# Kernel tuning notes

Measured on AMD Instinct MI355X. Metric: run time of the kernel, lower is better.

The kernel has to match this reference:

```python
import jax, jax.numpy as jnp
import numpy as np

T, D, H = 2048, 256, 256
DISCOUNT = 0.99
LAMBDA = 0.9
CONT_ALPHA = 0.01


def setup_inputs() -> dict:
    key = jax.random.key(0)
    ks = jax.random.split(key, 5)
    xs = jax.random.normal(ks[0], (T, D), jnp.float32)
    gs = jax.random.normal(ks[1], (T,), jnp.float32)            # returns / targets
    dones = (jax.random.uniform(ks[2], (T,)) < 0.02).astype(jnp.float32)  # sparse episode ends
    ys = jnp.stack([gs, dones], axis=1)                          # [T, 2] as in train_step
    W1 = jax.random.normal(ks[3], (D, H), jnp.float32) * (1.0 / float(np.sqrt(D)))
    b1 = jnp.zeros((H,), jnp.float32)
    W2 = jax.random.normal(ks[4], (H, 1), jnp.float32) * (1.0 / float(np.sqrt(H)))
    b2 = jnp.zeros((1,), jnp.float32)
    return {"xs": xs, "ys": ys, "W1": W1, "b1": b1, "W2": W2, "b2": b2}


def _value(params, x):
    # Value network: self(x)[0] for a batch of 1 -> scalar prediction.
    W1, b1, W2, b2 = params
    h = jax.nn.relu(x @ W1 + b1)          # [H]
    return (h @ W2 + b2)[0]               # scalar us


def _td_lambda(xs, ys, W1, b1, W2, b2):
    params = (W1, b1, W2, b2)
    gs, dones = ys[:, 0], ys[:, 1]
    zeros = tuple(jnp.zeros_like(p) for p in params)
    val_grad = jax.value_and_grad(_value)

    def step(carry, inp):
        z, total, r = carry
        x, g, done = inp
        us, grads = val_grad(params, x)   # grads of the PREDICTION us, as in tape.gradient(us, vars)
        error = (g - us) ** 2             # compiled_loss (MSE) on a single sample
        sigma = error - r                 # continuing TD error
        r = r + CONT_ALPHA * sigma
        # eligibility trace update and accumulated update
        z = tuple(DISCOUNT * LAMBDA * zi + gi for zi, gi in zip(z, grads))
        total = tuple(ti - sigma * zi for ti, zi in zip(total, z))
        # episode reset: zero traces and average-reward estimate when done
        keep = 1.0 - (done > 0.5).astype(jnp.float32)
        z = tuple(zi * keep for zi in z)
        r = r * keep
        return (z, total, r), sigma

    init = (zeros, zeros, jnp.float32(0.0))
    (_, total, _), sigmas = jax.lax.scan(step, init, (xs, gs, dones))
    # accumulated gradients for all trainable vars (flattened) + final sigma (reported loss)
    return jnp.concatenate([t.ravel() for t in total] + [sigmas[-1][None]])


def reference(xs, ys, W1, b1, W2, b2):
    return _td_lambda(xs, ys, W1, b1, W2, b2)
```

## Files before the change

kernel.cpp:

```cpp
#include <hip/hip_runtime.h>

#define GL  0.891f
#define OMA 0.99f
#define AL  0.01f

#define OFF_H   0
#define OFF_U   524288
#define OFF_PW1 526336
#define OFF_PB1 2623488
#define OFF_PW2 2631680
#define WS_FLOATS 2639872

__global__ __launch_bounds__(512, 2) void fwd_kernel(
    const float* __restrict__ xs, const float* __restrict__ W1,
    const float* __restrict__ b1, const float* __restrict__ W2,
    const float* __restrict__ b2,
    float* __restrict__ Hbuf, float* __restrict__ u) {
  const int tid = threadIdx.x;
  const int j = tid & 255;
  const int half = tid >> 8;
  const int r0 = blockIdx.x * 8;
  __shared__ __align__(16) float xsl[8 * 260];
  __shared__ __align__(16) float red[8][256];

  {
    const int row = tid >> 6;
    const int k0 = (tid & 63) * 4;
    float4 v = *reinterpret_cast<const float4*>(&xs[(r0 + row) * 256 + k0]);
    *reinterpret_cast<float4*>(&xsl[row * 260 + k0]) = v;
  }

  const int kb = half * 128;
  float wcur[16], wnxt[16];
#pragma unroll
  for (int kk = 0; kk < 16; ++kk)
    wcur[kk] = W1[(kb + kk) * 256 + j];
  __syncthreads();

  float acc[8] = {0.f, 0.f, 0.f, 0.f, 0.f, 0.f, 0.f, 0.f};
#pragma unroll
  for (int b = 0; b < 8; ++b) {
    if (b < 7) {
#pragma unroll
      for (int kk = 0; kk < 16; ++kk)
        wnxt[kk] = W1[(kb + (b + 1) * 16 + kk) * 256 + j];
    }
    const int k = kb + b * 16;
#pragma unroll
    for (int r = 0; r < 8; ++r) {
#pragma unroll
      for (int q = 0; q < 4; ++q) {
        const float4 xv = *reinterpret_cast<const float4*>(&xsl[r * 260 + k + 4 * q]);
        acc[r] = fmaf(xv.x, wcur[4 * q + 0], acc[r]);
        acc[r] = fmaf(xv.y, wcur[4 * q + 1], acc[r]);
        acc[r] = fmaf(xv.z, wcur[4 * q + 2], acc[r]);
        acc[r] = fmaf(xv.w, wcur[4 * q + 3], acc[r]);
      }
    }
#pragma unroll
    for (int kk = 0; kk < 16; ++kk) wcur[kk] = wnxt[kk];
  }

  if (half == 0) {
#pragma unroll
    for (int r = 0; r < 8; ++r) red[r][j] = acc[r];
  }
  __syncthreads();
  if (half == 1) {
    const float bj = b1[j];
    const float w2j = W2[j];
#pragma unroll
    for (int r = 0; r < 8; ++r) {
      const float a = red[r][j] + acc[r] + bj;
      const float h = fmaxf(a, 0.f);
      Hbuf[(r0 + r) * 256 + j] = h;
      red[r][j] = h * w2j;
    }
  }
  __syncthreads();
  for (int s = 128; s >= 1; s >>= 1) {
    if (j < s) {
#pragma unroll
      for (int rr = 0; rr < 4; ++rr)
        red[half * 4 + rr][j] += red[half * 4 + rr][j + s];
    }
    __syncthreads();
  }
  if (half == 0 && j < 8) u[r0 + j] = red[j][0] + b2[0];
}

__global__ __launch_bounds__(256, 4) void scan_w1_kernel(
    const float* __restrict__ u, const float* __restrict__ ys,
    const float* __restrict__ xs, const float* __restrict__ Hbuf,
    const float* __restrict__ W2,
    float* __restrict__ pW1, float* __restrict__ pB1, float* __restrict__ pW2,
    float* __restrict__ outp) {
  const int tid = threadIdx.x;
  const int blk = blockIdx.x;
  const int dc = blk >> 5;
  const int kc = blk & 31;
  const int d0 = dc * 32;
  const int tb = kc * 64;
  const int lane = tid & 63;
  const int w = tid >> 6;
  const int th = tid >> 7;
  const int j0 = tid & 127;
  const int tsl = th * 32;

  __shared__ __align__(16) float LDS[8704];
  float* xt = LDS;
  float* c_l = LDS + 2048;
  __shared__ float aggA[4], aggB[4], ag2A[4], ag2B[4], wsum[4];

#pragma unroll
  for (int q = 0; q < 2; ++q) {
    const int idx = tid * 2 + q;
    const int row = idx >> 3;
    const int qd = idx & 7;
    *reinterpret_cast<float4*>(&xt[row * 32 + qd * 4]) =
        *reinterpret_cast<const float4*>(&xs[(tb + row) * 256 + d0 + qd * 4]);
  }

  float hcur[16], hnxt[16];
#pragma unroll
  for (int i = 0; i < 8; ++i) {
    hcur[2 * i + 0] = Hbuf[(tb + tsl + i) * 256 + j0];
    hcur[2 * i + 1] = Hbuf[(tb + tsl + i) * 256 + j0 + 128];
  }

  float e[8], kp[8];
  {
    const float4 ua = ((const float4*)u)[2 * tid];
    const float4 ub = ((const float4*)u)[2 * tid + 1];
    const float uu[8] = {ua.x, ua.y, ua.z, ua.w, ub.x, ub.y, ub.z, ub.w};
#pragma unroll
    for (int q = 0; q < 4; ++q) {
      const float4 y = ((const float4*)ys)[4 * tid + q];
      float da = y.x - uu[2 * q];
      float db = y.z - uu[2 * q + 1];
      e[2 * q] = da * da;
      e[2 * q + 1] = db * db;
      kp[2 * q] = (y.y > 0.5f) ? 0.f : 1.f;
      kp[2 * q + 1] = (y.w > 0.5f) ? 0.f : 1.f;
    }
  }
  float A = 1.f, B = 0.f;
#pragma unroll
  for (int i = 0; i < 8; ++i) {
    const float a = kp[i] * OMA;
    B = fmaf(a, B, kp[i] * (AL * e[i]));
    A *= a;
  }
#pragma unroll
  for (int s = 1; s < 64; s <<= 1) {
    const float pA = __shfl_up(A, s, 64);
    const float pB = __shfl_up(B, s, 64);
    if (lane >= s) { B = fmaf(A, pB, B); A *= pA; }
  }
  if (lane == 63) { aggA[w] = A; aggB[w] = B; }
  __syncthreads();
  float rin;
  {
    float rw = 0.f;
    for (int v = 0; v < w; ++v) rw = fmaf(aggA[v], rw, aggB[v]);
    float lA = __shfl_up(A, 1, 64);
    float lB = __shfl_up(B, 1, 64);
    if (lane == 0) { lA = 1.f; lB = 0.f; }
    rin = fmaf(lA, rw, lB);
  }
  float sig[8];
  {
    float r = rin;
#pragma unroll
    for (int i = 0; i < 8; ++i) {
      sig[i] = e[i] - r;
      const float a = kp[i] * OMA;
      r = fmaf(a, r, kp[i] * (AL * e[i]));
    }
  }
  if (blk == 0 && tid == 255) outp[66049] = sig[7];

  float A2 = 1.f, B2 = 0.f;
#pragma unroll
  for (int i = 7; i >= 0; --i) {
    const float a = GL * kp[i];
    B2 = fmaf(a, B2, -sig[i]);
    A2 *= a;
  }
#pragma unroll
  for (int s = 1; s < 64; s <<= 1) {
    const float nA = __shfl_down(A2, s, 64);
    const float nB = __shfl_down(B2, s, 64);
    if (lane + s < 64) { B2 = fmaf(A2, nB, B2); A2 *= nA; }
  }
  if (lane == 0) { ag2A[w] = A2; ag2B[w] = B2; }
  __syncthreads();
  float cin;
  {
    float cw = 0.f;
    for (int v = 3; v > w; --v) cw = fmaf(ag2A[v], cw, ag2B[v]);
    float lA = __shfl_down(A2, 1, 64);
    float lB = __shfl_down(B2, 1, 64);
    if (lane == 63) { lA = 1.f; lB = 0.f; }
    cin = fmaf(lA, cw, lB);
  }
  float cr[8];
  float cc = cin, csum = 0.f;
#pragma unroll
  for (int i = 7; i >= 0; --i) {
    cc = fmaf(GL * kp[i], cc, -sig[i]);
    cr[i] = cc;
    csum += cc;
  }
  *reinterpret_cast<float4*>(&c_l[8 * tid]) = make_float4(cr[0], cr[1], cr[2], cr[3]);
  *reinterpret_cast<float4*>(&c_l[8 * tid + 4]) = make_float4(cr[4], cr[5], cr[6], cr[7]);
  if (blk == 0) {
#pragma unroll
    for (int s = 32; s >= 1; s >>= 1) csum += __shfl_xor(csum, s, 64);
    if (lane == 0) wsum[w] = csum;
  }
  __syncthreads();
  if (blk == 0 && tid == 0)
    outp[66048] = wsum[0] + wsum[1] + wsum[2] + wsum[3];

  const float w2a = W2[j0];
  const float w2b = W2[j0 + 128];
  float acc0[32], acc1[32];
#pragma unroll
  for (int d = 0; d < 32; ++d) { acc0[d] = 0.f; acc1[d] = 0.f; }
  float sb0 = 0.f, sb1 = 0.f, sw0 = 0.f, sw1 = 0.f;
  const bool do_bw = (dc == 0);

#pragma unroll
  for (int b = 0; b < 4; ++b) {
    if (b < 3) {
#pragma unroll
      for (int i = 0; i < 8; ++i) {
        hnxt[2 * i + 0] = Hbuf[(tb + tsl + (b + 1) * 8 + i) * 256 + j0];
        hnxt[2 * i + 1] = Hbuf[(tb + tsl + (b + 1) * 8 + i) * 256 + j0 + 128];
      }
    }
#pragma unroll
    for (int i = 0; i < 8; ++i) {
      const int tl = tsl + b * 8 + i;
      const float ct = c_l[tb + tl];
      const float h0 = hcur[2 * i + 0];
      const float h1 = hcur[2 * i + 1];
      const float gc0 = (h0 > 0.f) ? w2a * ct : 0.f;
      const float gc1 = (h1 > 0.f) ? w2b * ct : 0.f;
      if (do_bw) {
        sb0 += gc0; sb1 += gc1;
        sw0 = fmaf(ct, h0, sw0); sw1 = fmaf(ct, h1, sw1);
      }
#pragma unroll
      for (int q = 0; q < 8; ++q) {
        const float4 xv = *reinterpret_cast<const float4*>(&xt[tl * 32 + 4 * q]);
        acc0[4 * q + 0] = fmaf(gc0, xv.x, acc0[4 * q + 0]);
        acc0[4 * q + 1] = fmaf(gc0, xv.y, acc0[4 * q + 1]);
        acc0[4 * q + 2] = fmaf(gc0, xv.z, acc0[4 * q + 2]);
        acc0[4 * q + 3] = fmaf(gc0, xv.w, acc0[4 * q + 3]);
        acc1[4 * q + 0] = fmaf(gc1, xv.x, acc1[4 * q + 0]);
        acc1[4 * q + 1] = fmaf(gc1, xv.y, acc1[4 * q + 1]);
        acc1[4 * q + 2] = fmaf(gc1, xv.z, acc1[4 * q + 2]);
        acc1[4 * q + 3] = fmaf(gc1, xv.w, acc1[4 * q + 3]);
      }
    }
#pragma unroll
    for (int kk = 0; kk < 16; ++kk) hcur[kk] = hnxt[kk];
  }

  __syncthreads();
  if (th == 0) {
#pragma unroll
    for (int d = 0; d < 32; ++d) {
      LDS[(0 * 32 + d) * 128 + j0] = acc0[d];
      LDS[(32 + d) * 128 + j0] = acc1[d];
    }
    if (do_bw) {
      LDS[8192 + j0] = sb0;
      LDS[8192 + 128 + j0] = sb1;
      LDS[8448 + j0] = sw0;
      LDS[8448 + 128 + j0] = sw1;
    }
  }
  __syncthreads();
  if (th == 1) {
#pragma unroll
    for (int d = 0; d < 32; ++d) {
      pW1[kc * 65536 + (d0 + d) * 256 + j0] = LDS[d * 128 + j0] + acc0[d];
      pW1[kc * 65536 + (d0 + d) * 256 + j0 + 128] = LDS[(32 + d) * 128 + j0] + acc1[d];
    }
    if (do_bw) {
      pB1[kc * 256 + j0] = LDS[8192 + j0] + sb0;
      pB1[kc * 256 + j0 + 128] = LDS[8192 + 128 + j0] + sb1;
      pW2[kc * 256 + j0] = LDS[8448 + j0] + sw0;
      pW2[kc * 256 + j0 + 128] = LDS[8448 + 128 + j0] + sw1;
    }
  }
}

__global__ __launch_bounds__(256) void reduce_kernel(
    const float* __restrict__ pW1, const float* __restrict__ pB1,
    const float* __restrict__ pW2, float* __restrict__ outp) {
  if (blockIdx.x < 256) {
    const int col = blockIdx.x * 256 + threadIdx.x;
    float v[32];
#pragma unroll
    for (int k = 0; k < 32; ++k) v[k] = pW1[k * 65536 + col];
    float s = 0.f;
#pragma unroll
    for (int k = 0; k < 32; ++k) s += v[k];
    outp[col] = s;
  } else {
    const int j = threadIdx.x;
    float b[32], c[32];
#pragma unroll
    for (int k = 0; k < 32; ++k) { b[k] = pB1[k * 256 + j]; c[k] = pW2[k * 256 + j]; }
    float sb = 0.f, sw = 0.f;
#pragma unroll
    for (int k = 0; k < 32; ++k) { sb += b[k]; sw += c[k]; }
    outp[65536 + j] = sb;
    outp[65792 + j] = sw;
  }
}

extern "C" void kernel_launch(void* const* d_in, const int* in_sizes, int n_in,
                              void* d_out, int out_size, void* d_ws, size_t ws_size,
                              hipStream_t stream) {
  const float* xs = (const float*)d_in[0];
  const float* ys = (const float*)d_in[1];
  const float* W1 = (const float*)d_in[2];
  const float* b1 = (const float*)d_in[3];
  const float* W2 = (const float*)d_in[4];
  const float* b2 = (const float*)d_in[5];
  float* outp = (float*)d_out;
  float* ws = (float*)d_ws;

  if (ws_size < (size_t)WS_FLOATS * sizeof(float)) return;

  float* Hbuf = ws + OFF_H;
  float* ubuf = ws + OFF_U;
  float* pW1  = ws + OFF_PW1;
  float* pB1  = ws + OFF_PB1;
  float* pW2  = ws + OFF_PW2;

  fwd_kernel<<<256, 512, 0, stream>>>(xs, W1, b1, W2, b2, Hbuf, ubuf);
  scan_w1_kernel<<<256, 256, 0, stream>>>(ubuf, ys, xs, Hbuf, W2,
                                          pW1, pB1, pW2, outp);
  reduce_kernel<<<257, 256, 0, stream>>>(pW1, pB1, pW2, outp);
}
```

Baseline: 33.39 us.

## Repartition W1-gradient over output tiles and drop partial-sum reduce kernel

The scan/outer-product kernel now assigns each block a 16x16 tile of the W1 gradient and loops over all 2048 timesteps, instead of splitting time across blocks and writing 32 partial copies. The per-block results are reduced in-block with shuffles and LDS and written straight to the output. This removes the third reduce kernel and the large partial-sum workspace traffic. The cost is that every block reruns the full scan over all timesteps and streams xs and Hbuf over the whole time range from global memory without LDS staging.

```diff
diff --git a/kernel.cpp b/kernel.cpp
--- a/kernel.cpp
+++ b/kernel.cpp
@@ -4,12 +4,9 @@
 #define OMA 0.99f
 #define AL  0.01f
 
-#define OFF_H   0
-#define OFF_U   524288
-#define OFF_PW1 526336
-#define OFF_PB1 2623488
-#define OFF_PW2 2631680
-#define WS_FLOATS 2639872
+#define OFF_H 0
+#define OFF_U 524288
+#define WS_FLOATS 526336
 
 __global__ __launch_bounds__(512, 2) void fwd_kernel(
     const float* __restrict__ xs, const float* __restrict__ W1,
@@ -89,55 +86,41 @@
   if (half == 0 && j < 8) u[r0 + j] = red[j][0] + b2[0];
 }
 
-__global__ __launch_bounds__(256, 4) void scan_w1_kernel(
+__global__ __launch_bounds__(512, 2) void scan_w1_kernel(
     const float* __restrict__ u, const float* __restrict__ ys,
     const float* __restrict__ xs, const float* __restrict__ Hbuf,
-    const float* __restrict__ W2,
-    float* __restrict__ pW1, float* __restrict__ pB1, float* __restrict__ pW2,
-    float* __restrict__ outp) {
+    const float* __restrict__ W2, float* __restrict__ outp) {
   const int tid = threadIdx.x;
   const int blk = blockIdx.x;
-  const int dc = blk >> 5;
-  const int kc = blk & 31;
-  const int d0 = dc * 32;
-  const int tb = kc * 64;
+  const int dcb = blk >> 4;
+  const int jc = blk & 15;
+  const int d0 = dcb * 16;
+  const int j0 = jc * 16;
+  const int jj = tid & 15;
+  const int tt = tid >> 4;
   const int lane = tid & 63;
   const int w = tid >> 6;
-  const int th = tid >> 7;
-  const int j0 = tid & 127;
-  const int tsl = th * 32;
-
-  __shared__ __align__(16) float LDS[8704];
-  float* xt = LDS;
-  float* c_l = LDS + 2048;
-  __shared__ float aggA[4], aggB[4], ag2A[4], ag2B[4], wsum[4];
-
-#pragma unroll
-  for (int q = 0; q < 2; ++q) {
-    const int idx = tid * 2 + q;
-    const int row = idx >> 3;
-    const int qd = idx & 7;
-    *reinterpret_cast<float4*>(&xt[row * 32 + qd * 4]) =
-        *reinterpret_cast<const float4*>(&xs[(tb + row) * 256 + d0 + qd * 4]);
-  }
-
-  float hcur[16], hnxt[16];
-#pragma unroll
-  for (int i = 0; i < 8; ++i) {
-    hcur[2 * i + 0] = Hbuf[(tb + tsl + i) * 256 + j0];
-    hcur[2 * i + 1] = Hbuf[(tb + tsl + i) * 256 + j0 + 128];
-  }
-
-  float e[8], kp[8];
-  {
-    const float4 ua = ((const float4*)u)[2 * tid];
-    const float4 ub = ((const float4*)u)[2 * tid + 1];
-    const float uu[8] = {ua.x, ua.y, ua.z, ua.w, ub.x, ub.y, ub.z, ub.w};
-#pragma unroll
-    for (int q = 0; q < 4; ++q) {
-      const float4 y = ((const float4*)ys)[4 * tid + q];
-      float da = y.x - uu[2 * q];
-      float db = y.z - uu[2 * q + 1];
+
+  __shared__ __align__(16) float c_l[2048];
+  __shared__ float red[8][16][20];
+  __shared__ float aggA[8], aggB[8], ag2A[8], ag2B[8], wsum[8];
+
+  const float w2j = W2[j0 + jj];
+
+  float hA[8], hB[8];
+#pragma unroll
+  for (int i = 0; i < 8; ++i)
+    hA[i] = Hbuf[(i * 32 + tt) * 256 + j0 + jj];
+
+  float e[4], kp[4];
+  {
+    const float4 u4 = ((const float4*)u)[tid];
+    const float uu[4] = {u4.x, u4.y, u4.z, u4.w};
+#pragma unroll
+    for (int q = 0; q < 2; ++q) {
+      const float4 y = ((const float4*)ys)[2 * tid + q];
+      const float da = y.x - uu[2 * q];
+      const float db = y.z - uu[2 * q + 1];
       e[2 * q] = da * da;
       e[2 * q + 1] = db * db;
       kp[2 * q] = (y.y > 0.5f) ? 0.f : 1.f;
@@ -146,7 +129,7 @@
   }
   float A = 1.f, B = 0.f;
 #pragma unroll
-  for (int i = 0; i < 8; ++i) {
+  for (int i = 0; i < 4; ++i) {
     const float a = kp[i] * OMA;
     B = fmaf(a, B, kp[i] * (AL * e[i]));
     A *= a;
@@ -168,21 +151,21 @@
     if (lane == 0) { lA = 1.f; lB = 0.f; }
     rin = fmaf(lA, rw, lB);
   }
-  float sig[8];
+  float sig[4];
   {
     float r = rin;
 #pragma unroll
-    for (int i = 0; i < 8; ++i) {
+    for (int i = 0; i < 4; ++i) {
       sig[i] = e[i] - r;
       const float a = kp[i] * OMA;
       r = fmaf(a, r, kp[i] * (AL * e[i]));
     }
   }
-  if (blk == 0 && tid == 255) outp[66049] = sig[7];
+  if (blk == 0 && tid == 511) outp[66049] = sig[3];
 
   float A2 = 1.f, B2 = 0.f;
 #pragma unroll
-  for (int i = 7; i >= 0; --i) {
+  for (int i = 3; i >= 0; --i) {
     const float a = GL * kp[i];
     B2 = fmaf(a, B2, -sig[i]);
     A2 *= a;
@@ -198,129 +181,111 @@
   float cin;
   {
     float cw = 0.f;
-    for (int v = 3; v > w; --v) cw = fmaf(ag2A[v], cw, ag2B[v]);
+    for (int v = 7; v > w; --v) cw = fmaf(ag2A[v], cw, ag2B[v]);
     float lA = __shfl_down(A2, 1, 64);
     float lB = __shfl_down(B2, 1, 64);
     if (lane == 63) { lA = 1.f; lB = 0.f; }
     cin = fmaf(lA, cw, lB);
   }
-  float cr[8];
+  float cr[4];
   float cc = cin, csum = 0.f;
 #pragma unroll
-  for (int i = 7; i >= 0; --i) {
+  for (int i = 3; i >= 0; --i) {
     cc = fmaf(GL * kp[i], cc, -sig[i]);
     cr[i] = cc;
     csum += cc;
   }
-  *reinterpret_cast<float4*>(&c_l[8 * tid]) = make_float4(cr[0], cr[1], cr[2], cr[3]);
-  *reinterpret_cast<float4*>(&c_l[8 * tid + 4]) = make_float4(cr[4], cr[5], cr[6], cr[7]);
+  *reinterpret_cast<float4*>(&c_l[4 * tid]) = make_float4(cr[0], cr[1], cr[2], cr[3]);
   if (blk == 0) {
 #pragma unroll
     for (int s = 32; s >= 1; s >>= 1) csum += __shfl_xor(csum, s, 64);
     if (lane == 0) wsum[w] = csum;
   }
   __syncthreads();
-  if (blk == 0 && tid == 0)
-    outp[66048] = wsum[0] + wsum[1] + wsum[2] + wsum[3];
-
-  const float w2a = W2[j0];
-  const float w2b = W2[j0 + 128];
-  float acc0[32], acc1[32];
-#pragma unroll
-  for (int d = 0; d < 32; ++d) { acc0[d] = 0.f; acc1[d] = 0.f; }
-  float sb0 = 0.f, sb1 = 0.f, sw0 = 0.f, sw1 = 0.f;
-  const bool do_bw = (dc == 0);
-
-#pragma unroll
-  for (int b = 0; b < 4; ++b) {
-    if (b < 3) {
-#pragma unroll
-      for (int i = 0; i < 8; ++i) {
-        hnxt[2 * i + 0] = Hbuf[(tb + tsl + (b + 1) * 8 + i) * 256 + j0];
-        hnxt[2 * i + 1] = Hbuf[(tb + tsl + (b + 1) * 8 + i) * 256 + j0 + 128];
-      }
+  if (blk == 0 && tid == 0) {
+    float s = 0.f;
+#pragma unroll
+    for (int v = 0; v < 8; ++v) s += wsum[v];
+    outp[66048] = s;
+  }
+
+  float acc[16];
+#pragma unroll
+  for (int d = 0; d < 16; ++d) acc[d] = 0.f;
+  float sb = 0.f, sw = 0.f;
+  const bool do_bw = (dcb == 0);
+
+#pragma unroll 1
+  for (int cchunk = 0; cchunk < 8; ++cchunk) {
+    const int tc = cchunk * 256;
+    if (cchunk < 7) {
+#pragma unroll
+      for (int i = 0; i < 8; ++i)
+        hB[i] = Hbuf[(tc + 256 + i * 32 + tt) * 256 + j0 + jj];
     }
 #pragma unroll
     for (int i = 0; i < 8; ++i) {
-      const int tl = tsl + b * 8 + i;
-      const float ct = c_l[tb + tl];
-      const float h0 = hcur[2 * i + 0];
-      const float h1 = hcur[2 * i + 1];
-      const float gc0 = (h0 > 0.f) ? w2a * ct : 0.f;
-      const float gc1 = (h1 > 0.f) ? w2b * ct : 0.f;
-      if (do_bw) {
-        sb0 += gc0; sb1 += gc1;
-        sw0 = fmaf(ct, h0, sw0); sw1 = fmaf(ct, h1, sw1);
-      }
-#pragma unroll
-      for (int q = 0; q < 8; ++q) {
-        const float4 xv = *reinterpret_cast<const float4*>(&xt[tl * 32 + 4 * q]);
-        acc0[4 * q + 0] = fmaf(gc0, xv.x, acc0[4 * q + 0]);
-        acc0[4 * q + 1] = fmaf(gc0, xv.y, acc0[4 * q + 1]);
-        acc0[4 * q + 2] = fmaf(gc0, xv.z, acc0[4 * q + 2]);
-        acc0[4 * q + 3] = fmaf(gc0, xv.w, acc0[4 * q + 3]);
-        acc1[4 * q + 0] = fmaf(gc1, xv.x, acc1[4 * q + 0]);
-        acc1[4 * q + 1] = fmaf(gc1, xv.y, acc1[4 * q + 1]);
-        acc1[4 * q + 2] = fmaf(gc1, xv.z, acc1[4 * q + 2]);
-        acc1[4 * q + 3] = fmaf(gc1, xv.w, acc1[4 * q + 3]);
-      }
-    }
-#pragma unroll
-    for (int kk = 0; kk < 16; ++kk) hcur[kk] = hnxt[kk];
-  }
-
-  __syncthreads();
-  if (th == 0) {
-#pragma unroll
-    for (int d = 0; d < 32; ++d) {
-      LDS[(0 * 32 + d) * 128 + j0] = acc0[d];
-      LDS[(32 + d) * 128 + j0] = acc1[d];
-    }
-    if (do_bw) {
-      LDS[8192 + j0] = sb0;
-      LDS[8192 + 128 + j0] = sb1;
-      LDS[8448 + j0] = sw0;
-      LDS[8448 + 128 + j0] = sw1;
-    }
-  }
-  __syncthreads();
-  if (th == 1) {
-#pragma unroll
-    for (int d = 0; d < 32; ++d) {
-      pW1[kc * 65536 + (d0 + d) * 256 + j0] = LDS[d * 128 + j0] + acc0[d];
-      pW1[kc * 65536 + (d0 + d) * 256 + j0 + 128] = LDS[(32 + d) * 128 + j0] + acc1[d];
-    }
-    if (do_bw) {
-      pB1[kc * 256 + j0] = LDS[8192 + j0] + sb0;
-      pB1[kc * 256 + j0 + 128] = LDS[8192 + 128 + j0] + sb1;
-      pW2[kc * 256 + j0] = LDS[8448 + j0] + sw0;
-      pW2[kc * 256 + j0 + 128] = LDS[8448 + 128 + j0] + sw1;
-    }
-  }
-}
-
-__global__ __launch_bounds__(256) void reduce_kernel(
-    const float* __restrict__ pW1, const float* __restrict__ pB1,
-    const float* __restrict__ pW2, float* __restrict__ outp) {
-  if (blockIdx.x < 256) {
-    const int col = blockIdx.x * 256 + threadIdx.x;
-    float v[32];
-#pragma unroll
-    for (int k = 0; k < 32; ++k) v[k] = pW1[k * 65536 + col];
+      const int t = tc + i * 32 + tt;
+      const float ct = c_l[t];
+      const float h = hA[i];
+      const float gc = (h > 0.f) ? w2j * ct : 0.f;
+      if (do_bw) { sb += gc; sw = fmaf(ct, h, sw); }
+      const float* xp = &xs[t * 256 + d0];
+      const float4 x0 = *reinterpret_cast<const float4*>(xp);
+      const float4 x1 = *reinterpret_cast<const float4*>(xp + 4);
+      const float4 x2 = *reinterpret_cast<const float4*>(xp + 8);
+      const float4 x3 = *reinterpret_cast<const float4*>(xp + 12);
+      acc[0]  = fmaf(gc, x0.x, acc[0]);
+      acc[1]  = fmaf(gc, x0.y, acc[1]);
+      acc[2]  = fmaf(gc, x0.z, acc[2]);
+      acc[3]  = fmaf(gc, x0.w, acc[3]);
+      acc[4]  = fmaf(gc, x1.x, acc[4]);
+      acc[5]  = fmaf(gc, x1.y, acc[5]);
+      acc[6]  = fmaf(gc, x1.z, acc[6]);
+      acc[7]  = fmaf(gc, x1.w, acc[7]);
+      acc[8]  = fmaf(gc, x2.x, acc[8]);
+      acc[9]  = fmaf(gc, x2.y, acc[9]);
+      acc[10] = fmaf(gc, x2.z, acc[10]);
+      acc[11] = fmaf(gc, x2.w, acc[11]);
+      acc[12] = fmaf(gc, x3.x, acc[12]);
+      acc[13] = fmaf(gc, x3.y, acc[13]);
+      acc[14] = fmaf(gc, x3.z, acc[14]);
+      acc[15] = fmaf(gc, x3.w, acc[15]);
+    }
+#pragma unroll
+    for (int i = 0; i < 8; ++i) hA[i] = hB[i];
+  }
+
+#pragma unroll
+  for (int d = 0; d < 16; ++d) {
+    acc[d] += __shfl_xor(acc[d], 16, 64);
+    acc[d] += __shfl_xor(acc[d], 32, 64);
+  }
+  if (do_bw) {
+    sb += __shfl_xor(sb, 16, 64); sb += __shfl_xor(sb, 32, 64);
+    sw += __shfl_xor(sw, 16, 64); sw += __shfl_xor(sw, 32, 64);
+  }
+  if (lane < 16) {
+#pragma unroll
+    for (int d = 0; d < 16; ++d) red[w][lane][d] = acc[d];
+    if (do_bw) { red[w][lane][16] = sb; red[w][lane][17] = sw; }
+  }
+  __syncthreads();
+  if (tid < 256) {
+    const int oj = tid & 15;
+    const int od = tid >> 4;
     float s = 0.f;
 #pragma unroll
-    for (int k = 0; k < 32; ++k) s += v[k];
-    outp[col] = s;
-  } else {
-    const int j = threadIdx.x;
-    float b[32], c[32];
-#pragma unroll
-    for (int k = 0; k < 32; ++k) { b[k] = pB1[k * 256 + j]; c[k] = pW2[k * 256 + j]; }
-    float sb = 0.f, sw = 0.f;
-#pragma unroll
-    for (int k = 0; k < 32; ++k) { sb += b[k]; sw += c[k]; }
-    outp[65536 + j] = sb;
-    outp[65792 + j] = sw;
+    for (int v = 0; v < 8; ++v) s += red[v][oj][od];
+    outp[(d0 + od) * 256 + j0 + oj] = s;
+  } else if (do_bw && tid < 288) {
+    const int q = tid - 256;
+    const int col = q & 15;
+    const int sel = q >> 4;
+    float s = 0.f;
+#pragma unroll
+    for (int v = 0; v < 8; ++v) s += red[v][col][16 + sel];
+    outp[(sel ? 65792 : 65536) + j0 + col] = s;
   }
 }
 
@@ -340,12 +305,7 @@
 
   float* Hbuf = ws + OFF_H;
   float* ubuf = ws + OFF_U;
-  float* pW1  = ws + OFF_PW1;
-  float* pB1  = ws + OFF_PB1;
-  float* pW2  = ws + OFF_PW2;
 
   fwd_kernel<<<256, 512, 0, stream>>>(xs, W1, b1, W2, b2, Hbuf, ubuf);
-  scan_w1_kernel<<<256, 256, 0, stream>>>(ubuf, ys, xs, Hbuf, W2,
-                                          pW1, pB1, pW2, outp);
-  reduce_kernel<<<257, 256, 0, stream>>>(pW1, pB1, pW2, outp);
+  scan_w1_kernel<<<256, 512, 0, stream>>>(ubuf, ys, xs, Hbuf, W2, outp);
 }
```

Measured after the change: 34.68 us. 3.9% more time.
